# Kernel tuning notes

Hardware: AMD Instinct MI355X
Metric: run time of the kernel (lower is better)

## Reference

```python
import jax, jax.numpy as jnp
import numpy as np

B, S, D, H = 4, 2048, 1024, 16
DK = D // H


def setup_inputs() -> dict:
    key = jax.random.key(0)
    ks = jax.random.split(key, 9)
    x = jax.random.normal(ks[0], (B, S, D), dtype=jnp.float32)
    scale = 1.0 / np.sqrt(D)
    wq = jax.random.normal(ks[1], (D, D), dtype=jnp.float32) * scale
    wk = jax.random.normal(ks[2], (D, D), dtype=jnp.float32) * scale
    wv = jax.random.normal(ks[3], (D, D), dtype=jnp.float32) * scale
    wo = jax.random.normal(ks[4], (D, D), dtype=jnp.float32) * scale
    bq = jax.random.normal(ks[5], (D,), dtype=jnp.float32) * 0.01
    bk = jax.random.normal(ks[6], (D,), dtype=jnp.float32) * 0.01
    bv = jax.random.normal(ks[7], (D,), dtype=jnp.float32) * 0.01
    bo = jax.random.normal(ks[8], (D,), dtype=jnp.float32) * 0.01
    # causal mask: True where scores should be masked to -inf (j > i)
    mask = jnp.triu(jnp.ones((S, S), dtype=bool), k=1)[None, None, :, :]
    return {"x": x, "wq": wq, "bq": bq, "wk": wk, "bk": bk,
            "wv": wv, "bv": bv, "wo": wo, "bo": bo, "mask": mask}


def reference(x, wq, bq, wk, bk, wv, bv, wo, bo, mask):
    b, s, _ = x.shape
    # projections
    q = (x @ wq + bq).reshape(b, s, H, DK).transpose(0, 2, 1, 3)  # [B,H,S,DK]
    k = (x @ wk + bk).reshape(b, s, H, DK).transpose(0, 2, 1, 3)
    v = (x @ wv + bv).reshape(b, s, H, DK).transpose(0, 2, 1, 3)
    scores = jnp.einsum("bhqd,bhkd->bhqk", q, k) / np.sqrt(DK)
    scores = jnp.where(mask, -jnp.inf, scores)
    attn = jax.nn.softmax(scores, axis=-1)  # dropout p=0.0 -> identity
    out = jnp.einsum("bhqk,bhkd->bhqd", attn, v)
    out = out.transpose(0, 2, 1, 3).reshape(b, s, D)
    return out @ wo + bo
```

## Files before the change

kernel.cpp:

```cpp
#include <hip/hip_runtime.h>


typedef __attribute__((ext_vector_type(8))) short short8;
typedef __attribute__((ext_vector_type(4))) float floatx4;
typedef __attribute__((ext_vector_type(4))) unsigned short ushort4v;

#define SCLF (0.125f * 1.44269504f)

__device__ __forceinline__ unsigned short f2bf(float f) {
    unsigned int u = __float_as_uint(f);
    unsigned int r = (u + 0x7fffu + ((u >> 16) & 1u)) >> 16;
    return (unsigned short)r;
}

__device__ __forceinline__ unsigned int pk2bf(float lo, float hi) {
    return __builtin_amdgcn_perm(__float_as_uint(hi), __float_as_uint(lo), 0x07060302u);
}

__device__ __forceinline__ void gll16(const unsigned short* g, unsigned short* l) {
    __builtin_amdgcn_global_load_lds(
        (const __attribute__((address_space(1))) unsigned int*)g,
        (__attribute__((address_space(3))) unsigned int*)l, 16, 0, 0);
}

__device__ __forceinline__ void xcd_tile2(int nx, int& my, int& mx) {
    int lid = blockIdx.y * nx + blockIdx.x;
    int grp = lid & 7;
    int inner = lid >> 3;
    int m_per = (gridDim.y + 7) >> 3;
    my = grp * m_per + inner / nx;
    mx = inner % nx;
}

__global__ void cvtx_kernel(const float* __restrict__ x, unsigned short* __restrict__ xb) {
    int i = (blockIdx.x * 256 + threadIdx.x) * 4;
    float4 v = *(const float4*)&x[i];
    ushort4v o;
    o.x = f2bf(v.x); o.y = f2bf(v.y); o.z = f2bf(v.z); o.w = f2bf(v.w);
    *(ushort4v*)&xb[i] = o;
}

__global__ void wtrans_kernel(const float* __restrict__ wq, const float* __restrict__ wk,
                              const float* __restrict__ wv, const float* __restrict__ wo,
                              unsigned short* __restrict__ wtbase) {
    __shared__ float t[32][33];
    int z = blockIdx.z;
    const float* w = (z == 0) ? wq : (z == 1) ? wk : (z == 2) ? wv : wo;
    unsigned short* wt = wtbase + ((long)z << 20);
    int kb = blockIdx.y * 32, nb = blockIdx.x * 32;
    int col = threadIdx.x & 31, rw = threadIdx.x >> 5;
#pragma unroll
    for (int i = 0; i < 4; i++) {
        int row = rw + i * 8;
        t[row][col] = w[(kb + row) * 1024 + nb + col];
    }
    __syncthreads();
#pragma unroll
    for (int i = 0; i < 4; i++) {
        int row = rw + i * 8;
        wt[(nb + row) * 1024 + kb + col] = f2bf(t[col][row]);
    }
}

#define ASZ (256 * 64)
#define BSZ (128 * 64)

__device__ __forceinline__ short8 ldsr(const unsigned short* p) { return *(const short8*)p; }

template <bool SW>
__device__ __forceinline__ void gemm_core256(const unsigned short* __restrict__ A,
                                             const unsigned short* __restrict__ Bt,
                                             unsigned short* As, unsigned short* Bs,
                                             int m0, int n0, floatx4 (&acc)[8][2]) {
    const int K = 1024, NT = 16;
    int tid = threadIdx.x;
    int lane = tid & 63, wave = tid >> 6;
    int wm = wave >> 2, wn = wave & 3;
    int quad = lane >> 4, l15 = lane & 15, l7 = l15 & 7;
    int rsub = lane >> 3;
    int gl = (lane & 7) ^ rsub;

    floatx4 zero4 = {0.f, 0.f, 0.f, 0.f};
#pragma unroll
    for (int i = 0; i < 8; i++)
#pragma unroll
        for (int j = 0; j < 2; j++) acc[i][j] = zero4;

    auto stage = [&](int kt, int buf) {
        const unsigned short* Ag = A + (long)m0 * K + kt * 64;
        const unsigned short* Bg = Bt + (long)n0 * K + kt * 64;
        unsigned short* as = As + buf * ASZ;
        unsigned short* bs = Bs + buf * BSZ;
#pragma unroll
        for (int p = 0; p < 4; p++) {
            int chunk = wave * 4 + p;
            gll16(&Ag[(chunk * 8 + rsub) * K + gl * 8], &as[chunk * 512 + lane * 8]);
        }
#pragma unroll
        for (int p = 0; p < 2; p++) {
            int chunk = wave * 2 + p;
            gll16(&Bg[(chunk * 8 + rsub) * K + gl * 8], &bs[chunk * 512 + lane * 8]);
        }
    };

    stage(0, 0);
    stage(1, 1);
    asm volatile("s_waitcnt vmcnt(6)" ::: "memory");
    __builtin_amdgcn_s_barrier();
    asm volatile("" ::: "memory");

    for (int kt = 0; kt < NT; kt++) {
        int buf = kt & 1;
        const unsigned short* as = As + buf * ASZ;
        const unsigned short* bs = Bs + buf * BSZ;
        short8 bf[2][2], af[4][2], ag[4][2];
#pragma unroll
        for (int j = 0; j < 2; j++) {
            int rb = wn * 32 + j * 16 + l15;
#pragma unroll
            for (int kk = 0; kk < 2; kk++)
                bf[j][kk] = ldsr(&bs[rb * 64 + (((kk * 4 + quad) ^ l7) * 8)]);
        }
#pragma unroll
        for (int i = 0; i < 4; i++) {
            int r = wm * 128 + i * 16 + l15;
#pragma unroll
            for (int kk = 0; kk < 2; kk++)
                af[i][kk] = ldsr(&as[r * 64 + (((kk * 4 + quad) ^ l7) * 8)]);
        }
        __builtin_amdgcn_s_setprio(1);
#pragma unroll
        for (int i = 0; i < 4; i++)
#pragma unroll
            for (int j = 0; j < 2; j++)
#pragma unroll
                for (int kk = 0; kk < 2; kk++)
                    acc[i][j] = SW
                        ? __builtin_amdgcn_mfma_f32_16x16x32_bf16(bf[j][kk], af[i][kk], acc[i][j], 0, 0, 0)
                        : __builtin_amdgcn_mfma_f32_16x16x32_bf16(af[i][kk], bf[j][kk], acc[i][j], 0, 0, 0);
        __builtin_amdgcn_s_setprio(0);
#pragma unroll
        for (int i = 0; i < 4; i++) {
            int r = wm * 128 + 64 + i * 16 + l15;
#pragma unroll
            for (int kk = 0; kk < 2; kk++)
                ag[i][kk] = ldsr(&as[r * 64 + (((kk * 4 + quad) ^ l7) * 8)]);
        }
        __builtin_amdgcn_s_setprio(1);
#pragma unroll
        for (int i = 0; i < 4; i++)
#pragma unroll
            for (int j = 0; j < 2; j++)
#pragma unroll
                for (int kk = 0; kk < 2; kk++)
                    acc[4 + i][j] = SW
                        ? __builtin_amdgcn_mfma_f32_16x16x32_bf16(bf[j][kk], ag[i][kk], acc[4 + i][j], 0, 0, 0)
                        : __builtin_amdgcn_mfma_f32_16x16x32_bf16(ag[i][kk], bf[j][kk], acc[4 + i][j], 0, 0, 0);
        __builtin_amdgcn_s_setprio(0);
        asm volatile("" ::: "memory");
        __builtin_amdgcn_s_barrier();
        asm volatile("" ::: "memory");
        if (kt + 2 < NT) {
            stage(kt + 2, buf);
            asm volatile("s_waitcnt vmcnt(6)" ::: "memory");
        } else {
            asm volatile("s_waitcnt vmcnt(0)" ::: "memory");
        }
        __builtin_amdgcn_s_barrier();
        asm volatile("" ::: "memory");
    }
}

__global__ __launch_bounds__(512, 2) void proj_kernel(
    const unsigned short* __restrict__ xb, const unsigned short* __restrict__ wt,
    const float* __restrict__ bq, const float* __restrict__ bk, const float* __restrict__ bv,
    unsigned short* __restrict__ qo, unsigned short* __restrict__ ko,
    unsigned short* __restrict__ vo) {
    extern __shared__ __align__(16) unsigned short smem[];
    unsigned short* As = smem;
    unsigned short* Bs = smem + 2 * ASZ;
    int my, mx;
    xcd_tile2(24, my, mx);
    int m0 = my * 256, n0 = mx * 128;
    int tid = threadIdx.x, lane = tid & 63, wave = tid >> 6;
    int wm = wave >> 2, wn = wave & 3, quad = lane >> 4, l15 = lane & 15;
    floatx4 acc[8][2];

    if (n0 < 2048) {
        gemm_core256<true>(xb, wt, As, Bs, m0, n0, acc);
        int which = n0 >> 10;
        const float* bias = which ? bk : bq;
        unsigned short* dst = which ? ko : qo;
        float sc = which ? 1.0f : SCLF;
#pragma unroll
        for (int mt = 0; mt < 8; mt++)
#pragma unroll
            for (int nt = 0; nt < 2; nt++) {
                int tok = m0 + wm * 128 + mt * 16 + l15;
                int b = tok >> 11, s = tok & 2047;
                int colf = (n0 + wn * 32 + nt * 16 + quad * 4) & 1023;
                float4 bb = *(const float4*)&bias[colf];
                int h = colf >> 6, dk = colf & 63;
                ushort4v o;
                o.x = f2bf((acc[mt][nt][0] + bb.x) * sc);
                o.y = f2bf((acc[mt][nt][1] + bb.y) * sc);
                o.z = f2bf((acc[mt][nt][2] + bb.z) * sc);
                o.w = f2bf((acc[mt][nt][3] + bb.w) * sc);
                *(ushort4v*)&dst[((long)((b * 16 + h) * 2048 + s)) * 64 + dk] = o;
            }
    } else {
        gemm_core256<false>(xb, wt, As, Bs, m0, n0, acc);
#pragma unroll
        for (int mt = 0; mt < 8; mt++)
#pragma unroll
            for (int nt = 0; nt < 2; nt++) {
                int tok0 = m0 + wm * 128 + mt * 16 + quad * 4;
                int b = tok0 >> 11, s = tok0 & 2047;
                int colf = (n0 & 1023) + wn * 32 + nt * 16 + l15;
                int h = colf >> 6, dk = colf & 63;
                float bb = bv[colf];
                ushort4v o;
                o.x = f2bf(acc[mt][nt][0] + bb);
                o.y = f2bf(acc[mt][nt][1] + bb);
                o.z = f2bf(acc[mt][nt][2] + bb);
                o.w = f2bf(acc[mt][nt][3] + bb);
                *(ushort4v*)&vo[((long)((b * 16 + h) * 64 + dk)) * 2048 + s] = o;
            }
    }
}

__global__ __launch_bounds__(512, 2) void gemm_out_kernel(
    const unsigned short* __restrict__ ob, const unsigned short* __restrict__ wto,
    const float* __restrict__ bo, float* __restrict__ out) {
    extern __shared__ __align__(16) unsigned short smem[];
    unsigned short* As = smem;
    unsigned short* Bs = smem + 2 * ASZ;
    int my, mx;
    xcd_tile2(8, my, mx);
    int m0 = my * 256, n0 = mx * 128;
    int tid = threadIdx.x, lane = tid & 63, wave = tid >> 6;
    int wm = wave >> 2, wn = wave & 3, quad = lane >> 4, l15 = lane & 15;
    floatx4 acc[8][2];
    gemm_core256<true>(ob, wto, As, Bs, m0, n0, acc);

#pragma unroll
    for (int mt = 0; mt < 8; mt++)
#pragma unroll
        for (int nt = 0; nt < 2; nt++) {
            int tok = m0 + wm * 128 + mt * 16 + l15;
            int cg = n0 + wn * 32 + nt * 16 + quad * 4;
            float4 bb = *(const float4*)&bo[cg];
            float4 o;
            o.x = acc[mt][nt][0] + bb.x;
            o.y = acc[mt][nt][1] + bb.y;
            o.z = acc[mt][nt][2] + bb.z;
            o.w = acc[mt][nt][3] + bb.w;
            *(float4*)&out[(long)tok * 1024 + cg] = o;
        }
}

__device__ __forceinline__ void stage_kv(const unsigned short* __restrict__ Kg,
                                         const unsigned short* __restrict__ Vg,
                                         unsigned short* Ks, unsigned short* Vs,
                                         int lane, int wave) {
    int rsub = lane >> 3;
    int g = (lane & 7) ^ rsub;
#pragma unroll
    for (int p = 0; p < 2; p++) {
        int chunk = wave * 2 + p;
        int r = chunk * 8 + rsub;
        gll16(&Kg[r * 64 + g * 8], &Ks[chunk * 512]);
        gll16(&Vg[r * 2048 + g * 8], &Vs[chunk * 512]);
    }
}

__global__ __launch_bounds__(256, 4) void attn_kernel(
    const unsigned short* __restrict__ Q, const unsigned short* __restrict__ Kk,
    const unsigned short* __restrict__ Vt, unsigned short* __restrict__ O) {
    __shared__ __align__(16) unsigned short Ks[2][8 * 512];
    __shared__ __align__(16) unsigned short Vs[2][8 * 512];
    __shared__ __align__(16) unsigned short Ps[4 * 16 * 64];

    int bid = blockIdx.x;
    int qt = 15 - (bid >> 6);
    int bh = bid & 63;
    int q0 = qt * 128;
    long base = (long)bh * 2048 * 64;
    long vbase = (long)bh * 64 * 2048;
    int tid = threadIdx.x, lane = tid & 63, wave = tid >> 6;
    int quad = lane >> 4, l15 = lane & 15, l7 = l15 & 7;

    short8 qfA[2], qfB[2];
    int qrA = q0 + wave * 16 + l15;
    int qrB = qrA + 64;
    qfA[0] = *(const short8*)&Q[base + qrA * 64 + quad * 8];
    qfA[1] = *(const short8*)&Q[base + qrA * 64 + 32 + quad * 8];
    qfB[0] = *(const short8*)&Q[base + qrB * 64 + quad * 8];
    qfB[1] = *(const short8*)&Q[base + qrB * 64 + 32 + quad * 8];

    float lA = 0.f, lB = 0.f;
    floatx4 oA[4], oB[4];
    floatx4 zero4 = {0.f, 0.f, 0.f, 0.f};
#pragma unroll
    for (int st = 0; st < 4; st++) { oA[st] = zero4; oB[st] = zero4; }

    unsigned short* myP = &Ps[(wave * 16) * 64];
    int pw_off = l15 * 64 + (quad & 1) * 4;
    int pr0 = l15 * 64 + ((quad ^ l7) * 8);
    int pr1 = l15 * 64 + (((4 + quad) ^ l7) * 8);

    int ktmax = 2 * qt + 1;
    stage_kv(&Kk[base], &Vt[vbase], Ks[0], Vs[0], lane, wave);
    __syncthreads();

    for (int kt = 0; kt <= ktmax; kt++) {
        int cur = kt & 1;
        if (kt < ktmax)
            stage_kv(&Kk[base + (long)(kt + 1) * 64 * 64], &Vt[vbase + (kt + 1) * 64],
                     Ks[cur ^ 1], Vs[cur ^ 1], lane, wave);
        bool doA = (kt < ktmax);
        bool maskA = (kt == ktmax - 1);
        bool maskB = (kt == ktmax);

        floatx4 saA[4], saB[4];
#pragma unroll
        for (int st = 0; st < 4; st++) {
            int row = st * 16 + l15;
            short8 kf0 = ldsr(&Ks[cur][row * 64 + ((quad ^ l7) * 8)]);
            short8 kf1 = ldsr(&Ks[cur][row * 64 + (((4 + quad) ^ l7) * 8)]);
            saB[st] = __builtin_amdgcn_mfma_f32_16x16x32_bf16(kf0, qfB[0], zero4, 0, 0, 0);
            saB[st] = __builtin_amdgcn_mfma_f32_16x16x32_bf16(kf1, qfB[1], saB[st], 0, 0, 0);
            if (doA) {
                saA[st] = __builtin_amdgcn_mfma_f32_16x16x32_bf16(kf0, qfA[0], zero4, 0, 0, 0);
                saA[st] = __builtin_amdgcn_mfma_f32_16x16x32_bf16(kf1, qfA[1], saA[st], 0, 0, 0);
            }
        }

        int kg0 = kt * 64 + quad * 4;
        short8 pfB0, pfB1, pfA0, pfA1;
        {
            float p[4][4];
#pragma unroll
            for (int st = 0; st < 4; st++)
#pragma unroll
                for (int r = 0; r < 4; r++)
                    p[st][r] = __builtin_amdgcn_exp2f(saB[st][r]);
            if (maskB) {
#pragma unroll
                for (int st = 0; st < 4; st++)
#pragma unroll
                    for (int r = 0; r < 4; r++)
                        if (kg0 + st * 16 + r > qrB) p[st][r] = 0.f;
            }
            float rs = 0.f;
#pragma unroll
            for (int st = 0; st < 4; st++) {
                rs += p[st][0] + p[st][1] + p[st][2] + p[st][3];
                uint2 pw;
                pw.x = pk2bf(p[st][0], p[st][1]);
                pw.y = pk2bf(p[st][2], p[st][3]);
                *(uint2*)&myP[pw_off + (((st * 2 + (quad >> 1)) ^ l7) * 8)] = pw;
            }
            rs += __shfl_xor(rs, 16, 64);
            rs += __shfl_xor(rs, 32, 64);
            lB += rs;
            pfB0 = ldsr(&myP[pr0]);
            pfB1 = ldsr(&myP[pr1]);
        }
        if (doA) {
            float p[4][4];
#pragma unroll
            for (int st = 0; st < 4; st++)
#pragma unroll
                for (int r = 0; r < 4; r++)
                    p[st][r] = __builtin_amdgcn_exp2f(saA[st][r]);
            if (maskA) {
#pragma unroll
                for (int st = 0; st < 4; st++)
#pragma unroll
                    for (int r = 0; r < 4; r++)
                        if (kg0 + st * 16 + r > qrA) p[st][r] = 0.f;
            }
            float rs = 0.f;
#pragma unroll
            for (int st = 0; st < 4; st++) {
                rs += p[st][0] + p[st][1] + p[st][2] + p[st][3];
                uint2 pw;
                pw.x = pk2bf(p[st][0], p[st][1]);
                pw.y = pk2bf(p[st][2], p[st][3]);
                *(uint2*)&myP[pw_off + (((st * 2 + (quad >> 1)) ^ l7) * 8)] = pw;
            }
            rs += __shfl_xor(rs, 16, 64);
            rs += __shfl_xor(rs, 32, 64);
            lA += rs;
            pfA0 = ldsr(&myP[pr0]);
            pfA1 = ldsr(&myP[pr1]);
        }

#pragma unroll
        for (int st = 0; st < 4; st++) {
            int row = st * 16 + l15;
            short8 vf0 = ldsr(&Vs[cur][row * 64 + ((quad ^ l7) * 8)]);
            short8 vf1 = ldsr(&Vs[cur][row * 64 + (((4 + quad) ^ l7) * 8)]);
            oB[st] = __builtin_amdgcn_mfma_f32_16x16x32_bf16(vf0, pfB0, oB[st], 0, 0, 0);
            oB[st] = __builtin_amdgcn_mfma_f32_16x16x32_bf16(vf1, pfB1, oB[st], 0, 0, 0);
            if (doA) {
                oA[st] = __builtin_amdgcn_mfma_f32_16x16x32_bf16(vf0, pfA0, oA[st], 0, 0, 0);
                oA[st] = __builtin_amdgcn_mfma_f32_16x16x32_bf16(vf1, pfA1, oA[st], 0, 0, 0);
            }
        }
        __syncthreads();
    }

    int b = bh >> 4, h = bh & 15;
    float invA = 1.f / lA, invB = 1.f / lB;
#pragma unroll
    for (int st = 0; st < 4; st++) {
        uint2 ov;
        ov.x = pk2bf(oA[st][0] * invA, oA[st][1] * invA);
        ov.y = pk2bf(oA[st][2] * invA, oA[st][3] * invA);
        *(uint2*)&O[((long)(b * 2048 + qrA)) * 1024 + h * 64 + st * 16 + quad * 4] = ov;
        uint2 ow;
        ow.x = pk2bf(oB[st][0] * invB, oB[st][1] * invB);
        ow.y = pk2bf(oB[st][2] * invB, oB[st][3] * invB);
        *(uint2*)&O[((long)(b * 2048 + qrB)) * 1024 + h * 64 + st * 16 + quad * 4] = ow;
    }
}

extern "C" void kernel_launch(void* const* d_in, const int* in_sizes, int n_in,
                              void* d_out, int out_size, void* d_ws, size_t ws_size,
                              hipStream_t stream) {
    const float* x  = (const float*)d_in[0];
    const float* wq = (const float*)d_in[1];
    const float* bq = (const float*)d_in[2];
    const float* wk = (const float*)d_in[3];
    const float* bk = (const float*)d_in[4];
    const float* wv = (const float*)d_in[5];
    const float* bv = (const float*)d_in[6];
    const float* wo = (const float*)d_in[7];
    const float* bo = (const float*)d_in[8];

    char* w = (char*)d_ws;
    unsigned short* xb  = (unsigned short*)w;
    unsigned short* wtq = (unsigned short*)(w + (16u << 20));
    unsigned short* wto = wtq + (3u << 20);
    unsigned short* qb  = wto + (1u << 20);
    unsigned short* kb  = qb + (8u << 20);
    unsigned short* vb  = kb + (8u << 20);
    unsigned short* ob  = vb + (8u << 20);

    cvtx_kernel<<<8192, 256, 0, stream>>>(x, xb);
    wtrans_kernel<<<dim3(32, 32, 4), 256, 0, stream>>>(wq, wk, wv, wo, wtq);
    proj_kernel<<<dim3(24, 32), 512, 96 * 1024, stream>>>(xb, wtq, bq, bk, bv, qb, kb, vb);
    attn_kernel<<<1024, 256, 0, stream>>>(qb, kb, vb, ob);
    gemm_out_kernel<<<dim3(8, 32), 512, 96 * 1024, stream>>>(ob, wto, bo, (float*)d_out);
}
```

Baseline: 264.3 us.

## Triple-buffer GEMM LDS stages and remap tiles across XCDs

The shared GEMM core moves from double to triple buffering. It keeps A and B for each stage in one contiguous LDS region, prefetches three k-tiles ahead, and adjusts the vmcnt waits for the deeper pipeline. The block-to-tile mapping is also changed so that each XCD group covers four consecutive M tiles and iterates over N, which aims to improve L2 reuse. Dynamic LDS grows from 96 KB to 144 KB per block. That likely allows only one 512-thread block per CU instead of the two the launch bounds target, trading occupancy for more latency hiding.

```diff
diff --git a/kernel.cpp b/kernel.cpp
--- a/kernel.cpp
+++ b/kernel.cpp
@@ -23,13 +23,14 @@
         (__attribute__((address_space(3))) unsigned int*)l, 16, 0, 0);
 }
 
-__device__ __forceinline__ void xcd_tile2(int nx, int& my, int& mx) {
+__device__ __forceinline__ void xcd_tile3(int nx, int& m0, int& n0) {
     int lid = blockIdx.y * nx + blockIdx.x;
     int grp = lid & 7;
     int inner = lid >> 3;
-    int m_per = (gridDim.y + 7) >> 3;
-    my = grp * m_per + inner / nx;
-    mx = inner % nx;
+    int my = grp * 4 + (inner & 3);
+    int mx = inner >> 2;
+    m0 = my * 256;
+    n0 = mx * 128;
 }
 
 __global__ void cvtx_kernel(const float* __restrict__ x, unsigned short* __restrict__ xb) {
@@ -64,13 +65,14 @@
 
 #define ASZ (256 * 64)
 #define BSZ (128 * 64)
+#define BUFSZ (ASZ + BSZ)
 
 __device__ __forceinline__ short8 ldsr(const unsigned short* p) { return *(const short8*)p; }
 
 template <bool SW>
 __device__ __forceinline__ void gemm_core256(const unsigned short* __restrict__ A,
                                              const unsigned short* __restrict__ Bt,
-                                             unsigned short* As, unsigned short* Bs,
+                                             unsigned short* lds,
                                              int m0, int n0, floatx4 (&acc)[8][2]) {
     const int K = 1024, NT = 16;
     int tid = threadIdx.x;
@@ -86,11 +88,11 @@
 #pragma unroll
         for (int j = 0; j < 2; j++) acc[i][j] = zero4;
 
-    auto stage = [&](int kt, int buf) {
+    auto stage = [&](int kt, int b) {
         const unsigned short* Ag = A + (long)m0 * K + kt * 64;
         const unsigned short* Bg = Bt + (long)n0 * K + kt * 64;
-        unsigned short* as = As + buf * ASZ;
-        unsigned short* bs = Bs + buf * BSZ;
+        unsigned short* as = lds + b * BUFSZ;
+        unsigned short* bs = as + ASZ;
 #pragma unroll
         for (int p = 0; p < 4; p++) {
             int chunk = wave * 4 + p;
@@ -105,14 +107,15 @@
 
     stage(0, 0);
     stage(1, 1);
-    asm volatile("s_waitcnt vmcnt(6)" ::: "memory");
+    stage(2, 2);
+    asm volatile("s_waitcnt vmcnt(12)" ::: "memory");
     __builtin_amdgcn_s_barrier();
     asm volatile("" ::: "memory");
 
+    int buf = 0;
     for (int kt = 0; kt < NT; kt++) {
-        int buf = kt & 1;
-        const unsigned short* as = As + buf * ASZ;
-        const unsigned short* bs = Bs + buf * BSZ;
+        const unsigned short* as = lds + buf * BUFSZ;
+        const unsigned short* bs = as + ASZ;
         short8 bf[2][2], af[4][2], ag[4][2];
 #pragma unroll
         for (int j = 0; j < 2; j++) {
@@ -160,14 +163,17 @@
         asm volatile("" ::: "memory");
         __builtin_amdgcn_s_barrier();
         asm volatile("" ::: "memory");
-        if (kt + 2 < NT) {
-            stage(kt + 2, buf);
+        if (kt + 3 < NT) {
+            stage(kt + 3, buf);
+            asm volatile("s_waitcnt vmcnt(12)" ::: "memory");
+        } else if (kt + 3 == NT) {
             asm volatile("s_waitcnt vmcnt(6)" ::: "memory");
-        } else {
+        } else if (kt + 2 == NT) {
             asm volatile("s_waitcnt vmcnt(0)" ::: "memory");
         }
         __builtin_amdgcn_s_barrier();
         asm volatile("" ::: "memory");
+        buf = (buf == 2) ? 0 : buf + 1;
     }
 }
 
@@ -177,17 +183,14 @@
     unsigned short* __restrict__ qo, unsigned short* __restrict__ ko,
     unsigned short* __restrict__ vo) {
     extern __shared__ __align__(16) unsigned short smem[];
-    unsigned short* As = smem;
-    unsigned short* Bs = smem + 2 * ASZ;
-    int my, mx;
-    xcd_tile2(24, my, mx);
-    int m0 = my * 256, n0 = mx * 128;
+    int m0, n0;
+    xcd_tile3(24, m0, n0);
     int tid = threadIdx.x, lane = tid & 63, wave = tid >> 6;
     int wm = wave >> 2, wn = wave & 3, quad = lane >> 4, l15 = lane & 15;
     floatx4 acc[8][2];
 
     if (n0 < 2048) {
-        gemm_core256<true>(xb, wt, As, Bs, m0, n0, acc);
+        gemm_core256<true>(xb, wt, smem, m0, n0, acc);
         int which = n0 >> 10;
         const float* bias = which ? bk : bq;
         unsigned short* dst = which ? ko : qo;
@@ -209,7 +212,7 @@
                 *(ushort4v*)&dst[((long)((b * 16 + h) * 2048 + s)) * 64 + dk] = o;
             }
     } else {
-        gemm_core256<false>(xb, wt, As, Bs, m0, n0, acc);
+        gemm_core256<false>(xb, wt, smem, m0, n0, acc);
 #pragma unroll
         for (int mt = 0; mt < 8; mt++)
 #pragma unroll
@@ -233,15 +236,12 @@
     const unsigned short* __restrict__ ob, const unsigned short* __restrict__ wto,
     const float* __restrict__ bo, float* __restrict__ out) {
     extern __shared__ __align__(16) unsigned short smem[];
-    unsigned short* As = smem;
-    unsigned short* Bs = smem + 2 * ASZ;
-    int my, mx;
-    xcd_tile2(8, my, mx);
-    int m0 = my * 256, n0 = mx * 128;
+    int m0, n0;
+    xcd_tile3(8, m0, n0);
     int tid = threadIdx.x, lane = tid & 63, wave = tid >> 6;
     int wm = wave >> 2, wn = wave & 3, quad = lane >> 4, l15 = lane & 15;
     floatx4 acc[8][2];
-    gemm_core256<true>(ob, wto, As, Bs, m0, n0, acc);
+    gemm_core256<true>(ob, wto, smem, m0, n0, acc);
 
 #pragma unroll
     for (int mt = 0; mt < 8; mt++)
@@ -451,7 +451,7 @@
 
     cvtx_kernel<<<8192, 256, 0, stream>>>(x, xb);
     wtrans_kernel<<<dim3(32, 32, 4), 256, 0, stream>>>(wq, wk, wv, wo, wtq);
-    proj_kernel<<<dim3(24, 32), 512, 96 * 1024, stream>>>(xb, wtq, bq, bk, bv, qb, kb, vb);
+    proj_kernel<<<dim3(24, 32), 512, 144 * 1024, stream>>>(xb, wtq, bq, bk, bv, qb, kb, vb);
     attn_kernel<<<1024, 256, 0, stream>>>(qb, kb, vb, ob);
-    gemm_out_kernel<<<dim3(8, 32), 512, 96 * 1024, stream>>>(ob, wto, bo, (float*)d_out);
-}
+    gemm_out_kernel<<<dim3(8, 32), 512, 144 * 1024, stream>>>(ob, wto, bo, (float*)d_out);
+}
```

Result: no change. 265.8 us (+0.6%).
